# Kernel optimization log

Hardware: AMD Instinct MI355X
Metric: run time of the kernel (lower is better)

The kernel has to match this reference:

```python
import jax, jax.numpy as jnp
import numpy as np

B, T = 4, 2048
N_EMBD = 1024
TIME_EMBD = 128
N_HEAD = 16
C_IN = N_EMBD + TIME_EMBD  # 1152


def setup_inputs() -> dict:
    key = jax.random.key(0)
    ks = jax.random.split(key, 7)
    s_in = 1.0 / np.sqrt(C_IN)
    s_e = 1.0 / np.sqrt(N_EMBD)
    return {
        "x": jax.random.normal(ks[0], (B, T, C_IN), jnp.float32),
        "ln_w": jnp.ones((C_IN,), jnp.float32),
        "ln_b": jnp.zeros((C_IN,), jnp.float32),
        "W_attn": jax.random.normal(ks[1], (C_IN, 3 * N_EMBD), jnp.float32) * s_in,
        "b_attn": jax.random.normal(ks[2], (3 * N_EMBD,), jnp.float32) * 0.01,
        "W_proj": jax.random.normal(ks[3], (N_EMBD, N_EMBD), jnp.float32) * s_e,
        "b_proj": jax.random.normal(ks[4], (N_EMBD,), jnp.float32) * 0.01,
    }


def _layernorm(x, w, b, eps=1e-5):
    mu = jnp.mean(x, axis=-1, keepdims=True)
    var = jnp.var(x, axis=-1, keepdims=True)
    return (x - mu) * jax.lax.rsqrt(var + eps) * w + b


def reference(x, ln_w, ln_b, W_attn, b_attn, W_proj, b_proj):
    h = _layernorm(x, ln_w, ln_b)                      # [B,T,C_IN]
    qkv = h @ W_attn + b_attn                          # [B,T,3*N_EMBD]
    q, k, v = jnp.split(qkv, 3, axis=-1)
    hd = N_EMBD // N_HEAD
    q = q.reshape(B, T, N_HEAD, hd).transpose(0, 2, 1, 3)  # [B,H,T,hd]
    k = k.reshape(B, T, N_HEAD, hd).transpose(0, 2, 1, 3)
    v = v.reshape(B, T, N_HEAD, hd).transpose(0, 2, 1, 3)
    att = jnp.einsum("bhqd,bhkd->bhqk", q, k) * (1.0 / np.sqrt(hd))
    mask = jnp.tril(jnp.ones((T, T), bool))
    att = jnp.where(mask, att, -jnp.inf)
    att = jax.nn.softmax(att, axis=-1)                 # dropout p=0 -> identity
    y = jnp.einsum("bhqk,bhkd->bhqd", att, v)          # [B,H,T,hd]
    y = y.transpose(0, 2, 1, 3).reshape(B, T, N_EMBD)
    return y @ W_proj + b_proj
```

## Files before the change

kernel.cpp:

```cpp
#include <hip/hip_runtime.h>
#include <hip/hip_bf16.h>

#define BB 4
#define TT 2048
#define C_IN 1152
#define NE 1024
#define NH 16
#define HD 64
#define MM (BB*TT)
#define N_QKV (3*NE)

typedef __attribute__((ext_vector_type(8))) short s16x8;
typedef __attribute__((ext_vector_type(4))) float f32x4;

static __device__ __forceinline__ unsigned short f2bf(float x) {
    unsigned int u = __float_as_uint(x);
    unsigned int r = (u + 0x7fffu + ((u >> 16) & 1u)) >> 16;
    return (unsigned short)r;
}

static __device__ __forceinline__ void async16(const void* g, void* l) {
    __builtin_amdgcn_global_load_lds((const __attribute__((address_space(1))) void*)g,
                                     (__attribute__((address_space(3))) void*)l, 16, 0, 0);
}

__global__ __launch_bounds__(256) void ln_kernel(const float* __restrict__ x,
                                                 const float* __restrict__ w,
                                                 const float* __restrict__ b,
                                                 unsigned short* __restrict__ h) {
    const int row = blockIdx.x;
    const float* xr = x + (size_t)row * C_IN;
    float s = 0.f, sq = 0.f;
    for (int i = threadIdx.x; i < C_IN; i += 256) {
        float v = xr[i];
        s += v; sq += v * v;
    }
    for (int off = 1; off < 64; off <<= 1) {
        s  += __shfl_xor(s, off, 64);
        sq += __shfl_xor(sq, off, 64);
    }
    __shared__ float red[2][4];
    const int wid = threadIdx.x >> 6, lane = threadIdx.x & 63;
    if (lane == 0) { red[0][wid] = s; red[1][wid] = sq; }
    __syncthreads();
    s  = red[0][0] + red[0][1] + red[0][2] + red[0][3];
    sq = red[1][0] + red[1][1] + red[1][2] + red[1][3];
    const float mu  = s * (1.f / C_IN);
    const float var = sq * (1.f / C_IN) - mu * mu;
    const float rs  = rsqrtf(var + 1e-5f);
    unsigned short* hr = h + (size_t)row * C_IN;
    for (int i = threadIdx.x; i < C_IN; i += 256) {
        float v = (xr[i] - mu) * rs * w[i] + b[i];
        hr[i] = f2bf(v);
    }
}

__global__ __launch_bounds__(256) void transpose_cast(const float* __restrict__ in,
                                                      unsigned short* __restrict__ out,
                                                      int K, int N) {
    __shared__ float tile[32][33];
    const int n0 = blockIdx.x * 32, k0 = blockIdx.y * 32;
    const int tx = threadIdx.x & 31, ty = threadIdx.x >> 5;
    for (int i = ty; i < 32; i += 8)
        tile[i][tx] = in[(size_t)(k0 + i) * N + n0 + tx];
    __syncthreads();
    for (int i = ty; i < 32; i += 8)
        out[(size_t)(n0 + i) * K + k0 + tx] = f2bf(tile[tx][i]);
}

#define ATT_SC 0.18033688011112042f

#define EP_STRIDE 136
template <int MODE>
__global__ __launch_bounds__(256) void gemm_bt(const unsigned short* __restrict__ A,
                                               const unsigned short* __restrict__ Bt,
                                               const float* __restrict__ bias,
                                               void* __restrict__ outp,
                                               unsigned short* __restrict__ kb,
                                               unsigned short* __restrict__ vt,
                                               int M, int N, int K) {
    __shared__ unsigned short smem[16384];
    unsigned short* As = smem;
    unsigned short* Bs = smem + 8192;
    const int tid = threadIdx.x;
    const int wid = tid >> 6, lane = tid & 63;
    const int wm = wid >> 1, wn = wid & 1;
    const int quad = lane >> 4, l16 = lane & 15;
    const int m0 = blockIdx.y * 128, n0 = blockIdx.x * 128;

    const int srow = wid * 32 + (lane >> 2);
    const int scol = (lane & 3) * 8;
    const unsigned short* gA = A  + (size_t)(m0 + srow) * K + scol;
    const unsigned short* gB = Bt + (size_t)(n0 + srow) * K + scol;
    const int lofs = (wid * 32) * 32;

    f32x4 acc[4][4] = {};

    async16(gA,          &As[lofs]);
    async16(gA + 16 * K, &As[lofs + 16 * 32]);
    async16(gB,          &Bs[lofs]);
    async16(gB + 16 * K, &Bs[lofs + 16 * 32]);

    const int nk = K >> 5;
    for (int kt = 0; kt < nk; kt++) {
        __syncthreads();
        const int cur = kt & 1;
        if (kt + 1 < nk) {
            const int kk = (kt + 1) << 5;
            const int nxt = (cur ^ 1) * 4096;
            async16(gA + kk,          &As[nxt + lofs]);
            async16(gA + kk + 16 * K, &As[nxt + lofs + 16 * 32]);
            async16(gB + kk,          &Bs[nxt + lofs]);
            async16(gB + kk + 16 * K, &Bs[nxt + lofs + 16 * 32]);
        }
        const int cb = cur * 4096;
        s16x8 af[4], bfb[4];
        for (int mi = 0; mi < 4; mi++)
            af[mi] = *(const s16x8*)&As[cb + (wm * 64 + mi * 16 + l16) * 32 + quad * 8];
        for (int ni = 0; ni < 4; ni++)
            bfb[ni] = *(const s16x8*)&Bs[cb + (wn * 64 + ni * 16 + l16) * 32 + quad * 8];
        for (int mi = 0; mi < 4; mi++)
            for (int ni = 0; ni < 4; ni++)
                acc[mi][ni] = __builtin_amdgcn_mfma_f32_16x16x32_bf16(af[mi], bfb[ni], acc[mi][ni], 0, 0, 0);
    }

    const int which0 = n0 >> 10;
    const float sc = (MODE == 0 && which0 == 0) ? ATT_SC : 1.0f;
    for (int ni = 0; ni < 4; ni++) {
        const float bv = bias[n0 + wn * 64 + ni * 16 + l16];
        for (int mi = 0; mi < 4; mi++)
            for (int r = 0; r < 4; r++)
                acc[mi][ni][r] = (acc[mi][ni][r] + bv) * sc;
    }

    if (MODE == 1) {
        for (int mi = 0; mi < 4; mi++) {
            const int mbase = m0 + wm * 64 + mi * 16 + quad * 4;
            for (int ni = 0; ni < 4; ni++) {
                const int n_g = n0 + wn * 64 + ni * 16 + l16;
                for (int r = 0; r < 4; r++)
                    ((float*)outp)[(size_t)(mbase + r) * N + n_g] = acc[mi][ni][r];
            }
        }
        return;
    }

    const int which = n0 >> 10;
    const int bb = m0 >> 11;
    const int mloc = m0 & 2047;
    unsigned short* T = smem;

    if (which < 2) {
        unsigned short* qk = (which == 0) ? (unsigned short*)outp : kb;
        for (int pass = 0; pass < 2; pass++) {
            __syncthreads();
            if (wm == pass) {
                for (int mi = 0; mi < 4; mi++)
                    for (int ni = 0; ni < 4; ni++) {
                        const int nl = wn * 64 + ni * 16 + l16;
                        for (int r = 0; r < 4; r++)
                            T[(mi * 16 + quad * 4 + r) * EP_STRIDE + nl] = f2bf(acc[mi][ni][r]);
                    }
            }
            __syncthreads();
            const int ml = tid >> 2, c = tid & 3;
            const int t  = mloc + pass * 64 + ml;
            const int nl0 = c * 32;
            const int hh = ((n0 & 1023) >> 6) + (nl0 >> 6);
            const int d0 = nl0 & 63;
            unsigned short* dst = qk + ((size_t)(bb * 16 + hh) * TT + t) * HD + d0;
            const unsigned short* src = &T[ml * EP_STRIDE + nl0];
            for (int u = 0; u < 4; u++)
                *(s16x8*)(dst + u * 8) = *(const s16x8*)(src + u * 8);
        }
    } else {
        for (int pass = 0; pass < 2; pass++) {
            __syncthreads();
            if (wn == pass) {
                for (int mi = 0; mi < 4; mi++)
                    for (int ni = 0; ni < 4; ni++) {
                        const int nlh = ni * 16 + l16;
                        const int mlb = wm * 64 + mi * 16 + quad * 4;
                        for (int r = 0; r < 4; r += 2) {
                            const unsigned int pk = (unsigned int)f2bf(acc[mi][ni][r]) |
                                                    ((unsigned int)f2bf(acc[mi][ni][r + 1]) << 16);
                            *(unsigned int*)&T[nlh * EP_STRIDE + mlb + r] = pk;
                        }
                    }
            }
            __syncthreads();
            const int nlh = tid >> 2, c = tid & 3;
            const int hh = (n0 - 2048 + pass * 64) >> 6;
            unsigned short* dst = vt + ((size_t)(bb * 16 + hh) * HD + nlh) * TT + mloc + c * 32;
            const unsigned short* src = &T[nlh * EP_STRIDE + c * 32];
            for (int u = 0; u < 4; u++)
                *(s16x8*)(dst + u * 8) = *(const s16x8*)(src + u * 8);
        }
    }
}

#define PST 72

__global__ __launch_bounds__(256) void attn_kernel(const unsigned short* __restrict__ qb,
                                                   const unsigned short* __restrict__ kb,
                                                   const unsigned short* __restrict__ vt,
                                                   unsigned short* __restrict__ yb) {
    __shared__ unsigned short Ks[2][64 * 64];
    __shared__ unsigned short Vs[2][64 * 64];
    __shared__ unsigned short Ps[4][2 * 16 * PST];
    const int tid = threadIdx.x, wid = tid >> 6, lane = tid & 63;
    const int quad = lane >> 4, l16 = lane & 15;
    const int bh = blockIdx.x & 63;
    const int qblk = 15 - (blockIdx.x >> 6);

    const unsigned short* qh = qb + (size_t)bh * TT * HD;
    const unsigned short* kh = kb + (size_t)bh * TT * HD;
    const unsigned short* vh = vt + (size_t)bh * HD * TT;
    unsigned short* ps = Ps[wid];

    const int q0w = qblk * 128 + wid * 32;
    s16x8 aq[2][2];
    #pragma unroll
    for (int mf = 0; mf < 2; mf++) {
        aq[mf][0] = *(const s16x8*)&qh[(size_t)(q0w + mf * 16 + l16) * HD + quad * 8];
        aq[mf][1] = *(const s16x8*)&qh[(size_t)(q0w + mf * 16 + l16) * HD + 32 + quad * 8];
    }
    s16x8 onesf;
    #pragma unroll
    for (int i = 0; i < 8; i++) onesf[i] = (short)0x3F80;

    f32x4 yacc[2][4] = {};
    f32x4 lacc[2] = {};
    const int ntiles = 2 * qblk + 2;

    const int rl = lane >> 3;
    const int cc = (lane & 7) ^ (rl & 7);
    const unsigned short* kp0 = kh + (size_t)(wid * 16 + rl) * HD + cc * 8;
    const unsigned short* kp1 = kh + (size_t)(wid * 16 + 8 + rl) * HD + cc * 8;
    const unsigned short* vp0 = vh + (size_t)(wid * 16 + rl) * TT + cc * 8;
    const unsigned short* vp1 = vh + (size_t)(wid * 16 + 8 + rl) * TT + cc * 8;
    const int ldsK0 = wid * 16 * 64, ldsK1 = (wid * 16 + 8) * 64;

    async16(kp0, &Ks[0][ldsK0]);  async16(kp1, &Ks[0][ldsK1]);
    async16(vp0, &Vs[0][ldsK0]);  async16(vp1, &Vs[0][ldsK1]);
    kp0 += 64 * HD; kp1 += 64 * HD; vp0 += 64; vp1 += 64;

    const int p0s = quad ^ (l16 & 7);
    const int p1s = (4 + quad) ^ (l16 & 7);

#define ATT_STEP(CUR, TT_)                                                              \
    {                                                                                   \
        __syncthreads();                                                                \
        if ((TT_) + 1 < ntiles) {                                                       \
            async16(kp0, &Ks[(CUR) ^ 1][ldsK0]);  async16(kp1, &Ks[(CUR) ^ 1][ldsK1]);  \
            async16(vp0, &Vs[(CUR) ^ 1][ldsK0]);  async16(vp1, &Vs[(CUR) ^ 1][ldsK1]);  \
            kp0 += 64 * HD; kp1 += 64 * HD; vp0 += 64; vp1 += 64;                       \
        }                                                                               \
        const int tk0 = (TT_) * 64;                                                     \
        if (tk0 <= q0w + 31) {                                                          \
            const unsigned short* Kc = Ks[CUR];                                         \
            const unsigned short* Vc = Vs[CUR];                                         \
            s16x8 kf[4][2], vf[4][2];                                                   \
            _Pragma("unroll")                                                           \
            for (int nj = 0; nj < 4; nj++) {                                            \
                kf[nj][0] = *(const s16x8*)&Kc[(nj * 16 + l16) * 64 + p0s * 8];         \
                kf[nj][1] = *(const s16x8*)&Kc[(nj * 16 + l16) * 64 + p1s * 8];         \
            }                                                                           \
            _Pragma("unroll")                                                           \
            for (int ni = 0; ni < 4; ni++) {                                            \
                vf[ni][0] = *(const s16x8*)&Vc[(ni * 16 + l16) * 64 + p0s * 8];         \
                vf[ni][1] = *(const s16x8*)&Vc[(ni * 16 + l16) * 64 + p1s * 8];         \
            }                                                                           \
            _Pragma("unroll")                                                           \
            for (int mf = 0; mf < 2; mf++) {                                            \
                const int f0 = q0w + mf * 16;                                           \
                if (tk0 > f0 + 15) continue;                                            \
                unsigned short* pm = ps + mf * (16 * PST);                              \
                const int qg = f0 + l16;                                                \
                f32x4 st[4];                                                            \
                _Pragma("unroll")                                                       \
                for (int nj = 0; nj < 4; nj++) {                                        \
                    f32x4 z = {};                                                       \
                    z = __builtin_amdgcn_mfma_f32_16x16x32_bf16(kf[nj][0], aq[mf][0], z, 0, 0, 0); \
                    z = __builtin_amdgcn_mfma_f32_16x16x32_bf16(kf[nj][1], aq[mf][1], z, 0, 0, 0); \
                    st[nj] = z;                                                         \
                }                                                                       \
                const bool diag = (tk0 + 64 > f0);                                      \
                _Pragma("unroll")                                                       \
                for (int nj = 0; nj < 4; nj++) {                                        \
                    const int keyb = tk0 + nj * 16 + quad * 4;                          \
                    float pv[4];                                                        \
                    _Pragma("unroll")                                                   \
                    for (int r = 0; r < 4; r++) {                                       \
                        float p = exp2f(st[nj][r]);                                     \
                        if (diag && (keyb + r > qg)) p = 0.f;                           \
                        pv[r] = p;                                                      \
                    }                                                                   \
                    const unsigned int pk0 = __builtin_amdgcn_perm(                     \
                        __float_as_uint(pv[1]), __float_as_uint(pv[0]), 0x07060302u);   \
                    const unsigned int pk1 = __builtin_amdgcn_perm(                     \
                        __float_as_uint(pv[3]), __float_as_uint(pv[2]), 0x07060302u);   \
                    *(uint2*)&pm[l16 * PST + nj * 16 + quad * 4] = make_uint2(pk0, pk1);\
                }                                                                       \
                __asm volatile("s_waitcnt lgkmcnt(0)" ::: "memory");                    \
                const s16x8 ap0 = *(const s16x8*)&pm[l16 * PST + quad * 8];             \
                const s16x8 ap1 = *(const s16x8*)&pm[l16 * PST + 32 + quad * 8];        \
                lacc[mf] = __builtin_amdgcn_mfma_f32_16x16x32_bf16(ap0, onesf, lacc[mf], 0, 0, 0); \
                lacc[mf] = __builtin_amdgcn_mfma_f32_16x16x32_bf16(ap1, onesf, lacc[mf], 0, 0, 0); \
                _Pragma("unroll")                                                       \
                for (int ni = 0; ni < 4; ni++) {                                        \
                    yacc[mf][ni] = __builtin_amdgcn_mfma_f32_16x16x32_bf16(ap0, vf[ni][0], yacc[mf][ni], 0, 0, 0); \
                    yacc[mf][ni] = __builtin_amdgcn_mfma_f32_16x16x32_bf16(ap1, vf[ni][1], yacc[mf][ni], 0, 0, 0); \
                }                                                                       \
            }                                                                           \
        }                                                                               \
    }

    for (int t = 0; t < ntiles; t += 2) {
        ATT_STEP(0, t);
        ATT_STEP(1, t + 1);
    }
#undef ATT_STEP

    const int bbi = bh >> 4, hh = bh & 15;
    #pragma unroll
    for (int mf = 0; mf < 2; mf++) {
        float linv[4];
        #pragma unroll
        for (int r = 0; r < 4; r++)
            linv[r] = 1.0f / lacc[mf][r];
        #pragma unroll
        for (int ni = 0; ni < 4; ni++)
            #pragma unroll
            for (int r = 0; r < 4; r++) {
                const int trow = q0w + mf * 16 + quad * 4 + r;
                yb[((size_t)bbi * TT + trow) * NE + hh * HD + ni * 16 + l16] =
                    f2bf(yacc[mf][ni][r] * linv[r]);
            }
    }
}

extern "C" void kernel_launch(void* const* d_in, const int* in_sizes, int n_in,
                              void* d_out, int out_size, void* d_ws, size_t ws_size,
                              hipStream_t stream) {
    const float* x      = (const float*)d_in[0];
    const float* ln_w   = (const float*)d_in[1];
    const float* ln_b   = (const float*)d_in[2];
    const float* W_attn = (const float*)d_in[3];
    const float* b_attn = (const float*)d_in[4];
    const float* W_proj = (const float*)d_in[5];
    const float* b_proj = (const float*)d_in[6];
    float* out = (float*)d_out;

    char* ws = (char*)d_ws;
    unsigned short* h    = (unsigned short*)ws;  ws += (size_t)MM * C_IN * 2;
    unsigned short* Wat  = (unsigned short*)ws;  ws += (size_t)N_QKV * C_IN * 2;
    unsigned short* Wpt  = (unsigned short*)ws;  ws += (size_t)NE * NE * 2;
    unsigned short* qbuf = (unsigned short*)ws;  ws += (size_t)MM * NE * 2;
    unsigned short* kbuf = (unsigned short*)ws;  ws += (size_t)MM * NE * 2;
    unsigned short* vtbf = (unsigned short*)ws;  ws += (size_t)MM * NE * 2;
    unsigned short* ybuf = (unsigned short*)ws;  ws += (size_t)MM * NE * 2;

    ln_kernel<<<MM, 256, 0, stream>>>(x, ln_w, ln_b, h);
    transpose_cast<<<dim3(N_QKV / 32, C_IN / 32), 256, 0, stream>>>(W_attn, Wat, C_IN, N_QKV);
    transpose_cast<<<dim3(NE / 32, NE / 32), 256, 0, stream>>>(W_proj, Wpt, NE, NE);
    gemm_bt<0><<<dim3(N_QKV / 128, MM / 128), 256, 0, stream>>>(h, Wat, b_attn, qbuf, kbuf, vtbf,
                                                                MM, N_QKV, C_IN);
    attn_kernel<<<64 * 16, 256, 0, stream>>>(qbuf, kbuf, vtbf, ybuf);
    gemm_bt<1><<<dim3(NE / 128, MM / 128), 256, 0, stream>>>(ybuf, Wpt, b_proj, out, nullptr, nullptr,
                                                             MM, NE, NE);
}
```

Before: 314.5 us.

## Replace GEMM with 256x256-tile, 512-thread kernel using a four-stage LDS ring

Both GEMMs move from a 128x128 tile with 256 threads and double buffering to a 256x256 tile with 8 waves. A four-slot LDS ring is filled two k-steps ahead, with explicit vmcnt waits and raw barriers in place of __syncthreads. LDS is laid out in MFMA fragment order so each lane reads contiguous 16-byte fragments, and the MFMA bursts are wrapped in s_setprio. The bias add and scaling move into the epilogue stores, which are widened to 256 columns. Each block now needs 128 KB of LDS, and the grids shrink to 384 and 128 blocks, which may leave CUs idle, especially in the output projection.

```diff
diff --git a/kernel.cpp b/kernel.cpp
--- a/kernel.cpp
+++ b/kernel.cpp
@@ -70,76 +70,96 @@
 
 #define ATT_SC 0.18033688011112042f
 
-#define EP_STRIDE 136
+#define EPAD 264
+
 template <int MODE>
-__global__ __launch_bounds__(256) void gemm_bt(const unsigned short* __restrict__ A,
-                                               const unsigned short* __restrict__ Bt,
-                                               const float* __restrict__ bias,
-                                               void* __restrict__ outp,
-                                               unsigned short* __restrict__ kb,
-                                               unsigned short* __restrict__ vt,
-                                               int M, int N, int K) {
-    __shared__ unsigned short smem[16384];
-    unsigned short* As = smem;
-    unsigned short* Bs = smem + 8192;
+__global__ __launch_bounds__(512, 2) void gemm_fm(const unsigned short* __restrict__ A,
+                                                  const unsigned short* __restrict__ Bt,
+                                                  const float* __restrict__ bias,
+                                                  void* __restrict__ outp,
+                                                  unsigned short* __restrict__ kb,
+                                                  unsigned short* __restrict__ vt,
+                                                  int M, int N, int K) {
+    __shared__ unsigned short sm[65536];
+    unsigned short* sA = sm;
+    unsigned short* sB = sm + 32768;
     const int tid = threadIdx.x;
-    const int wid = tid >> 6, lane = tid & 63;
-    const int wm = wid >> 1, wn = wid & 1;
+    const int lane = tid & 63, wid = tid >> 6;
+    const int wm = wid >> 2, wn = wid & 3;
     const int quad = lane >> 4, l16 = lane & 15;
-    const int m0 = blockIdx.y * 128, n0 = blockIdx.x * 128;
-
-    const int srow = wid * 32 + (lane >> 2);
-    const int scol = (lane & 3) * 8;
-    const unsigned short* gA = A  + (size_t)(m0 + srow) * K + scol;
-    const unsigned short* gB = Bt + (size_t)(n0 + srow) * K + scol;
-    const int lofs = (wid * 32) * 32;
-
-    f32x4 acc[4][4] = {};
-
-    async16(gA,          &As[lofs]);
-    async16(gA + 16 * K, &As[lofs + 16 * 32]);
-    async16(gB,          &Bs[lofs]);
-    async16(gB + 16 * K, &Bs[lofs + 16 * 32]);
-
+    const int m0 = blockIdx.y * 256, n0 = blockIdx.x * 256;
+
+    const unsigned short* gA0 = A  + (size_t)(m0 + wid * 16 + l16) * K + quad * 8;
+    const unsigned short* gB0 = Bt + (size_t)(n0 + wid * 16 + l16) * K + quad * 8;
+    const size_t j1 = (size_t)128 * K;
+    const int stA0 = wid * 512, stA1 = (8 + wid) * 512;
+
+    f32x4 acc[8][4] = {};
     const int nk = K >> 5;
-    for (int kt = 0; kt < nk; kt++) {
-        __syncthreads();
-        const int cur = kt & 1;
-        if (kt + 1 < nk) {
-            const int kk = (kt + 1) << 5;
-            const int nxt = (cur ^ 1) * 4096;
-            async16(gA + kk,          &As[nxt + lofs]);
-            async16(gA + kk + 16 * K, &As[nxt + lofs + 16 * 32]);
-            async16(gB + kk,          &Bs[nxt + lofs]);
-            async16(gB + kk + 16 * K, &Bs[nxt + lofs + 16 * 32]);
-        }
-        const int cb = cur * 4096;
-        s16x8 af[4], bfb[4];
+
+    async16(gA0,           &sA[stA0]);          async16(gA0 + j1,      &sA[stA1]);
+    async16(gB0,           &sB[stA0]);          async16(gB0 + j1,      &sB[stA1]);
+    async16(gA0 + 32,      &sA[8192 + stA0]);   async16(gA0 + j1 + 32, &sA[8192 + stA1]);
+    async16(gB0 + 32,      &sB[8192 + stA0]);   async16(gB0 + j1 + 32, &sB[8192 + stA1]);
+
+    for (int kt = 0; kt < nk; ++kt) {
+        const int cb = (kt & 3) * 8192;
+        if (kt + 1 < nk) { asm volatile("s_waitcnt vmcnt(4)" ::: "memory"); }
+        else             { asm volatile("s_waitcnt vmcnt(0)" ::: "memory"); }
+        __builtin_amdgcn_s_barrier();
+
+        const int pre = kt + 2;
+        const bool do_pre = (pre < nk);
+        const int pb = (pre & 3) * 8192;
+        const unsigned short* pA = gA0 + pre * 32;
+        const unsigned short* pB = gB0 + pre * 32;
+
+        s16x8 af[4], bf[4];
+        #pragma unroll
+        for (int i = 0; i < 4; i++)
+            af[i] = *(const s16x8*)&sA[cb + (wm * 8 + i) * 512 + lane * 8];
+        #pragma unroll
+        for (int i = 0; i < 4; i++)
+            bf[i] = *(const s16x8*)&sB[cb + (wn * 4 + i) * 512 + lane * 8];
+        if (do_pre) { async16(pA, &sA[pb + stA0]); async16(pA + j1, &sA[pb + stA1]); }
+        __builtin_amdgcn_s_setprio(1);
+        #pragma unroll
         for (int mi = 0; mi < 4; mi++)
-            af[mi] = *(const s16x8*)&As[cb + (wm * 64 + mi * 16 + l16) * 32 + quad * 8];
-        for (int ni = 0; ni < 4; ni++)
-            bfb[ni] = *(const s16x8*)&Bs[cb + (wn * 64 + ni * 16 + l16) * 32 + quad * 8];
+            #pragma unroll
+            for (int ni = 0; ni < 4; ni++)
+                acc[mi][ni] = __builtin_amdgcn_mfma_f32_16x16x32_bf16(af[mi], bf[ni], acc[mi][ni], 0, 0, 0);
+        __builtin_amdgcn_s_setprio(0);
+        __builtin_amdgcn_s_barrier();
+
+        #pragma unroll
+        for (int i = 0; i < 4; i++)
+            af[i] = *(const s16x8*)&sA[cb + (wm * 8 + 4 + i) * 512 + lane * 8];
+        if (do_pre) { async16(pB, &sB[pb + stA0]); async16(pB + j1, &sB[pb + stA1]); }
+        __builtin_amdgcn_s_setprio(1);
+        #pragma unroll
         for (int mi = 0; mi < 4; mi++)
+            #pragma unroll
             for (int ni = 0; ni < 4; ni++)
-                acc[mi][ni] = __builtin_amdgcn_mfma_f32_16x16x32_bf16(af[mi], bfb[ni], acc[mi][ni], 0, 0, 0);
-    }
-
-    const int which0 = n0 >> 10;
-    const float sc = (MODE == 0 && which0 == 0) ? ATT_SC : 1.0f;
-    for (int ni = 0; ni < 4; ni++) {
-        const float bv = bias[n0 + wn * 64 + ni * 16 + l16];
-        for (int mi = 0; mi < 4; mi++)
-            for (int r = 0; r < 4; r++)
-                acc[mi][ni][r] = (acc[mi][ni][r] + bv) * sc;
-    }
+                acc[4 + mi][ni] = __builtin_amdgcn_mfma_f32_16x16x32_bf16(af[mi], bf[ni], acc[4 + mi][ni], 0, 0, 0);
+        __builtin_amdgcn_s_setprio(0);
+    }
+
+    float bv[4];
+    #pragma unroll
+    for (int ni = 0; ni < 4; ni++)
+        bv[ni] = bias[n0 + wn * 64 + ni * 16 + l16];
 
     if (MODE == 1) {
-        for (int mi = 0; mi < 4; mi++) {
-            const int mbase = m0 + wm * 64 + mi * 16 + quad * 4;
+        float* out = (float*)outp;
+        #pragma unroll
+        for (int mf = 0; mf < 8; mf++) {
+            const int mg = m0 + wm * 128 + mf * 16 + quad * 4;
+            #pragma unroll
             for (int ni = 0; ni < 4; ni++) {
-                const int n_g = n0 + wn * 64 + ni * 16 + l16;
+                const int ng = n0 + wn * 64 + ni * 16 + l16;
+                #pragma unroll
                 for (int r = 0; r < 4; r++)
-                    ((float*)outp)[(size_t)(mbase + r) * N + n_g] = acc[mi][ni][r];
+                    out[(size_t)(mg + r) * N + ng] = acc[mf][ni][r] + bv[ni];
             }
         }
         return;
@@ -148,53 +168,65 @@
     const int which = n0 >> 10;
     const int bb = m0 >> 11;
     const int mloc = m0 & 2047;
-    unsigned short* T = smem;
+    const float sc = (which == 0) ? ATT_SC : 1.0f;
+    unsigned short* T = sm;
 
     if (which < 2) {
         unsigned short* qk = (which == 0) ? (unsigned short*)outp : kb;
-        for (int pass = 0; pass < 2; pass++) {
+        const int hb = (n0 & 1023) >> 6;
+        for (int p = 0; p < 4; p++) {
             __syncthreads();
-            if (wm == pass) {
-                for (int mi = 0; mi < 4; mi++)
+            if (wm == (p >> 1)) {
+                #pragma unroll
+                for (int i = 0; i < 4; i++) {
+                    const int mf = (p & 1) * 4 + i;
+                    #pragma unroll
                     for (int ni = 0; ni < 4; ni++) {
-                        const int nl = wn * 64 + ni * 16 + l16;
+                        const int col = wn * 64 + ni * 16 + l16;
+                        #pragma unroll
                         for (int r = 0; r < 4; r++)
-                            T[(mi * 16 + quad * 4 + r) * EP_STRIDE + nl] = f2bf(acc[mi][ni][r]);
+                            T[(i * 16 + quad * 4 + r) * EPAD + col] =
+                                f2bf((acc[mf][ni][r] + bv[ni]) * sc);
                     }
+                }
             }
             __syncthreads();
-            const int ml = tid >> 2, c = tid & 3;
-            const int t  = mloc + pass * 64 + ml;
-            const int nl0 = c * 32;
-            const int hh = ((n0 & 1023) >> 6) + (nl0 >> 6);
-            const int d0 = nl0 & 63;
-            unsigned short* dst = qk + ((size_t)(bb * 16 + hh) * TT + t) * HD + d0;
-            const unsigned short* src = &T[ml * EP_STRIDE + nl0];
-            for (int u = 0; u < 4; u++)
-                *(s16x8*)(dst + u * 8) = *(const s16x8*)(src + u * 8);
+            const int c0 = (tid & 31) * 8;
+            const int hh = hb + (c0 >> 6), d0 = c0 & 63;
+            for (int rr = tid >> 5; rr < 64; rr += 16) {
+                const int t = mloc + p * 64 + rr;
+                *(s16x8*)(qk + ((size_t)(bb * 16 + hh) * TT + t) * HD + d0) =
+                    *(const s16x8*)&T[rr * EPAD + c0];
+            }
         }
     } else {
-        for (int pass = 0; pass < 2; pass++) {
+        const int hb = (n0 - 2048) >> 6;
+        for (int p = 0; p < 4; p++) {
             __syncthreads();
-            if (wn == pass) {
-                for (int mi = 0; mi < 4; mi++)
+            if (wn == p) {
+                #pragma unroll
+                for (int mf = 0; mf < 8; mf++) {
+                    const int colb = wm * 128 + mf * 16 + quad * 4;
+                    #pragma unroll
                     for (int ni = 0; ni < 4; ni++) {
-                        const int nlh = ni * 16 + l16;
-                        const int mlb = wm * 64 + mi * 16 + quad * 4;
-                        for (int r = 0; r < 4; r += 2) {
-                            const unsigned int pk = (unsigned int)f2bf(acc[mi][ni][r]) |
-                                                    ((unsigned int)f2bf(acc[mi][ni][r + 1]) << 16);
-                            *(unsigned int*)&T[nlh * EP_STRIDE + mlb + r] = pk;
-                        }
+                        const int rowt = ni * 16 + l16;
+                        const unsigned int pk0 =
+                            (unsigned int)f2bf(acc[mf][ni][0] + bv[ni]) |
+                            ((unsigned int)f2bf(acc[mf][ni][1] + bv[ni]) << 16);
+                        const unsigned int pk1 =
+                            (unsigned int)f2bf(acc[mf][ni][2] + bv[ni]) |
+                            ((unsigned int)f2bf(acc[mf][ni][3] + bv[ni]) << 16);
+                        *(unsigned int*)&T[rowt * EPAD + colb]     = pk0;
+                        *(unsigned int*)&T[rowt * EPAD + colb + 2] = pk1;
                     }
+                }
             }
             __syncthreads();
-            const int nlh = tid >> 2, c = tid & 3;
-            const int hh = (n0 - 2048 + pass * 64) >> 6;
-            unsigned short* dst = vt + ((size_t)(bb * 16 + hh) * HD + nlh) * TT + mloc + c * 32;
-            const unsigned short* src = &T[nlh * EP_STRIDE + c * 32];
-            for (int u = 0; u < 4; u++)
-                *(s16x8*)(dst + u * 8) = *(const s16x8*)(src + u * 8);
+            const int c0 = (tid & 31) * 8;
+            for (int dr = tid >> 5; dr < 64; dr += 16) {
+                *(s16x8*)(vt + ((size_t)(bb * 16 + hb + p) * HD + dr) * TT + mloc + c0) =
+                    *(const s16x8*)&T[dr * EPAD + c0];
+            }
         }
     }
 }
@@ -364,9 +396,9 @@
     ln_kernel<<<MM, 256, 0, stream>>>(x, ln_w, ln_b, h);
     transpose_cast<<<dim3(N_QKV / 32, C_IN / 32), 256, 0, stream>>>(W_attn, Wat, C_IN, N_QKV);
     transpose_cast<<<dim3(NE / 32, NE / 32), 256, 0, stream>>>(W_proj, Wpt, NE, NE);
-    gemm_bt<0><<<dim3(N_QKV / 128, MM / 128), 256, 0, stream>>>(h, Wat, b_attn, qbuf, kbuf, vtbf,
+    gemm_fm<0><<<dim3(N_QKV / 256, MM / 256), 512, 0, stream>>>(h, Wat, b_attn, qbuf, kbuf, vtbf,
                                                                 MM, N_QKV, C_IN);
     attn_kernel<<<64 * 16, 256, 0, stream>>>(qbuf, kbuf, vtbf, ybuf);
-    gemm_bt<1><<<dim3(NE / 128, MM / 128), 256, 0, stream>>>(ybuf, Wpt, b_proj, out, nullptr, nullptr,
+    gemm_fm<1><<<dim3(NE / 256, MM / 256), 512, 0, stream>>>(ybuf, Wpt, b_proj, out, nullptr, nullptr,
                                                              MM, NE, NE);
 }
```

Measured after the change: 375.6 us. 1.19x slower.

## Triple-buffer attention K/V loads, remap GEMM block order, raise MFMA priority

Applied to the files above, without the earlier changes.

Attention now keeps three K/V LDS buffers with two tiles prefetched ahead. Each step waits with an explicit vmcnt plus a raw s_barrier instead of __syncthreads, so global-load latency is better hidden behind compute. The P-matrix writes for both query fragments happen before the PV MFMAs, which run at raised wave priority. Separately, the GEMM remaps block IDs in an XCD-interleaved order to improve L2 locality across chiplets; the cost is more LDS per attention block, which may lower occupancy.

```diff
diff --git a/kernel.cpp b/kernel.cpp
--- a/kernel.cpp
+++ b/kernel.cpp
@@ -86,7 +86,12 @@
     const int wid = tid >> 6, lane = tid & 63;
     const int wm = wid >> 1, wn = wid & 1;
     const int quad = lane >> 4, l16 = lane & 15;
-    const int m0 = blockIdx.y * 128, n0 = blockIdx.x * 128;
+
+    const int gx  = gridDim.x;
+    const int nwg = gx * gridDim.y;
+    const int bid = blockIdx.y * gx + blockIdx.x;
+    const int wg  = (bid & 7) * (nwg >> 3) + (bid >> 3);
+    const int m0 = (wg / gx) * 128, n0 = (wg % gx) * 128;
 
     const int srow = wid * 32 + (lane >> 2);
     const int scol = (lane & 3) * 8;
@@ -205,8 +210,8 @@
                                                    const unsigned short* __restrict__ kb,
                                                    const unsigned short* __restrict__ vt,
                                                    unsigned short* __restrict__ yb) {
-    __shared__ unsigned short Ks[2][64 * 64];
-    __shared__ unsigned short Vs[2][64 * 64];
+    __shared__ unsigned short Ks[3][64 * 64];
+    __shared__ unsigned short Vs[3][64 * 64];
     __shared__ unsigned short Ps[4][2 * 16 * PST];
     const int tid = threadIdx.x, wid = tid >> 6, lane = tid & 63;
     const int quad = lane >> 4, l16 = lane & 15;
@@ -244,83 +249,89 @@
     async16(kp0, &Ks[0][ldsK0]);  async16(kp1, &Ks[0][ldsK1]);
     async16(vp0, &Vs[0][ldsK0]);  async16(vp1, &Vs[0][ldsK1]);
     kp0 += 64 * HD; kp1 += 64 * HD; vp0 += 64; vp1 += 64;
+    async16(kp0, &Ks[1][ldsK0]);  async16(kp1, &Ks[1][ldsK1]);
+    async16(vp0, &Vs[1][ldsK0]);  async16(vp1, &Vs[1][ldsK1]);
+    kp0 += 64 * HD; kp1 += 64 * HD; vp0 += 64; vp1 += 64;
 
     const int p0s = quad ^ (l16 & 7);
     const int p1s = (4 + quad) ^ (l16 & 7);
 
-#define ATT_STEP(CUR, TT_)                                                              \
-    {                                                                                   \
-        __syncthreads();                                                                \
-        if ((TT_) + 1 < ntiles) {                                                       \
-            async16(kp0, &Ks[(CUR) ^ 1][ldsK0]);  async16(kp1, &Ks[(CUR) ^ 1][ldsK1]);  \
-            async16(vp0, &Vs[(CUR) ^ 1][ldsK0]);  async16(vp1, &Vs[(CUR) ^ 1][ldsK1]);  \
-            kp0 += 64 * HD; kp1 += 64 * HD; vp0 += 64; vp1 += 64;                       \
-        }                                                                               \
-        const int tk0 = (TT_) * 64;                                                     \
-        if (tk0 <= q0w + 31) {                                                          \
-            const unsigned short* Kc = Ks[CUR];                                         \
-            const unsigned short* Vc = Vs[CUR];                                         \
-            s16x8 kf[4][2], vf[4][2];                                                   \
-            _Pragma("unroll")                                                           \
-            for (int nj = 0; nj < 4; nj++) {                                            \
-                kf[nj][0] = *(const s16x8*)&Kc[(nj * 16 + l16) * 64 + p0s * 8];         \
-                kf[nj][1] = *(const s16x8*)&Kc[(nj * 16 + l16) * 64 + p1s * 8];         \
-            }                                                                           \
-            _Pragma("unroll")                                                           \
-            for (int ni = 0; ni < 4; ni++) {                                            \
-                vf[ni][0] = *(const s16x8*)&Vc[(ni * 16 + l16) * 64 + p0s * 8];         \
-                vf[ni][1] = *(const s16x8*)&Vc[(ni * 16 + l16) * 64 + p1s * 8];         \
-            }                                                                           \
-            _Pragma("unroll")                                                           \
-            for (int mf = 0; mf < 2; mf++) {                                            \
-                const int f0 = q0w + mf * 16;                                           \
-                if (tk0 > f0 + 15) continue;                                            \
-                unsigned short* pm = ps + mf * (16 * PST);                              \
-                const int qg = f0 + l16;                                                \
-                f32x4 st[4];                                                            \
-                _Pragma("unroll")                                                       \
-                for (int nj = 0; nj < 4; nj++) {                                        \
-                    f32x4 z = {};                                                       \
-                    z = __builtin_amdgcn_mfma_f32_16x16x32_bf16(kf[nj][0], aq[mf][0], z, 0, 0, 0); \
-                    z = __builtin_amdgcn_mfma_f32_16x16x32_bf16(kf[nj][1], aq[mf][1], z, 0, 0, 0); \
-                    st[nj] = z;                                                         \
-                }                                                                       \
-                const bool diag = (tk0 + 64 > f0);                                      \
-                _Pragma("unroll")                                                       \
-                for (int nj = 0; nj < 4; nj++) {                                        \
-                    const int keyb = tk0 + nj * 16 + quad * 4;                          \
-                    float pv[4];                                                        \
-                    _Pragma("unroll")                                                   \
-                    for (int r = 0; r < 4; r++) {                                       \
-                        float p = exp2f(st[nj][r]);                                     \
-                        if (diag && (keyb + r > qg)) p = 0.f;                           \
-                        pv[r] = p;                                                      \
-                    }                                                                   \
-                    const unsigned int pk0 = __builtin_amdgcn_perm(                     \
-                        __float_as_uint(pv[1]), __float_as_uint(pv[0]), 0x07060302u);   \
-                    const unsigned int pk1 = __builtin_amdgcn_perm(                     \
-                        __float_as_uint(pv[3]), __float_as_uint(pv[2]), 0x07060302u);   \
-                    *(uint2*)&pm[l16 * PST + nj * 16 + quad * 4] = make_uint2(pk0, pk1);\
-                }                                                                       \
-                __asm volatile("s_waitcnt lgkmcnt(0)" ::: "memory");                    \
-                const s16x8 ap0 = *(const s16x8*)&pm[l16 * PST + quad * 8];             \
-                const s16x8 ap1 = *(const s16x8*)&pm[l16 * PST + 32 + quad * 8];        \
-                lacc[mf] = __builtin_amdgcn_mfma_f32_16x16x32_bf16(ap0, onesf, lacc[mf], 0, 0, 0); \
-                lacc[mf] = __builtin_amdgcn_mfma_f32_16x16x32_bf16(ap1, onesf, lacc[mf], 0, 0, 0); \
-                _Pragma("unroll")                                                       \
-                for (int ni = 0; ni < 4; ni++) {                                        \
-                    yacc[mf][ni] = __builtin_amdgcn_mfma_f32_16x16x32_bf16(ap0, vf[ni][0], yacc[mf][ni], 0, 0, 0); \
-                    yacc[mf][ni] = __builtin_amdgcn_mfma_f32_16x16x32_bf16(ap1, vf[ni][1], yacc[mf][ni], 0, 0, 0); \
-                }                                                                       \
-            }                                                                           \
-        }                                                                               \
-    }
-
-    for (int t = 0; t < ntiles; t += 2) {
-        ATT_STEP(0, t);
-        ATT_STEP(1, t + 1);
-    }
-#undef ATT_STEP
+    int bsel = 0;
+    for (int t = 0; t < ntiles; ++t) {
+        if (t + 1 < ntiles) { asm volatile("s_waitcnt vmcnt(4)" ::: "memory"); }
+        else                { asm volatile("s_waitcnt vmcnt(0)" ::: "memory"); }
+        __builtin_amdgcn_s_barrier();
+        if (t + 2 < ntiles) {
+            const int wsel = (bsel == 0) ? 2 : bsel - 1;
+            async16(kp0, &Ks[wsel][ldsK0]);  async16(kp1, &Ks[wsel][ldsK1]);
+            async16(vp0, &Vs[wsel][ldsK0]);  async16(vp1, &Vs[wsel][ldsK1]);
+            kp0 += 64 * HD; kp1 += 64 * HD; vp0 += 64; vp1 += 64;
+        }
+        const int tk0 = t * 64;
+        if (tk0 <= q0w + 31) {
+            const unsigned short* Kc = Ks[bsel];
+            const unsigned short* Vc = Vs[bsel];
+            s16x8 kf[4][2], vf[4][2];
+            #pragma unroll
+            for (int nj = 0; nj < 4; nj++) {
+                kf[nj][0] = *(const s16x8*)&Kc[(nj * 16 + l16) * 64 + p0s * 8];
+                kf[nj][1] = *(const s16x8*)&Kc[(nj * 16 + l16) * 64 + p1s * 8];
+            }
+            #pragma unroll
+            for (int ni = 0; ni < 4; ni++) {
+                vf[ni][0] = *(const s16x8*)&Vc[(ni * 16 + l16) * 64 + p0s * 8];
+                vf[ni][1] = *(const s16x8*)&Vc[(ni * 16 + l16) * 64 + p1s * 8];
+            }
+            #pragma unroll
+            for (int mf = 0; mf < 2; mf++) {
+                const int f0 = q0w + mf * 16;
+                unsigned short* pm = ps + mf * (16 * PST);
+                const int qg = f0 + l16;
+                f32x4 st[4];
+                #pragma unroll
+                for (int nj = 0; nj < 4; nj++) {
+                    f32x4 z = {};
+                    z = __builtin_amdgcn_mfma_f32_16x16x32_bf16(kf[nj][0], aq[mf][0], z, 0, 0, 0);
+                    z = __builtin_amdgcn_mfma_f32_16x16x32_bf16(kf[nj][1], aq[mf][1], z, 0, 0, 0);
+                    st[nj] = z;
+                }
+                const bool diag = (tk0 + 64 > f0);
+                #pragma unroll
+                for (int nj = 0; nj < 4; nj++) {
+                    const int keyb = tk0 + nj * 16 + quad * 4;
+                    float pv[4];
+                    #pragma unroll
+                    for (int r = 0; r < 4; r++) {
+                        float p = exp2f(st[nj][r]);
+                        if (diag && (keyb + r > qg)) p = 0.f;
+                        pv[r] = p;
+                    }
+                    const unsigned int pk0 = __builtin_amdgcn_perm(
+                        __float_as_uint(pv[1]), __float_as_uint(pv[0]), 0x07060302u);
+                    const unsigned int pk1 = __builtin_amdgcn_perm(
+                        __float_as_uint(pv[3]), __float_as_uint(pv[2]), 0x07060302u);
+                    *(uint2*)&pm[l16 * PST + nj * 16 + quad * 4] = make_uint2(pk0, pk1);
+                }
+            }
+            __asm volatile("s_waitcnt lgkmcnt(0)" ::: "memory");
+            __builtin_amdgcn_s_setprio(1);
+            #pragma unroll
+            for (int mf = 0; mf < 2; mf++) {
+                unsigned short* pm = ps + mf * (16 * PST);
+                const s16x8 ap0 = *(const s16x8*)&pm[l16 * PST + quad * 8];
+                const s16x8 ap1 = *(const s16x8*)&pm[l16 * PST + 32 + quad * 8];
+                lacc[mf] = __builtin_amdgcn_mfma_f32_16x16x32_bf16(ap0, onesf, lacc[mf], 0, 0, 0);
+                lacc[mf] = __builtin_amdgcn_mfma_f32_16x16x32_bf16(ap1, onesf, lacc[mf], 0, 0, 0);
+                #pragma unroll
+                for (int ni = 0; ni < 4; ni++) {
+                    yacc[mf][ni] = __builtin_amdgcn_mfma_f32_16x16x32_bf16(ap0, vf[ni][0], yacc[mf][ni], 0, 0, 0);
+                    yacc[mf][ni] = __builtin_amdgcn_mfma_f32_16x16x32_bf16(ap1, vf[ni][1], yacc[mf][ni], 0, 0, 0);
+                }
+            }
+            __builtin_amdgcn_s_setprio(0);
+        }
+        bsel = (bsel == 2) ? 0 : bsel + 1;
+    }
 
     const int bbi = bh >> 4, hh = bh & 15;
     #pragma unroll
```

Measured after the change: 310.6 us. About the same (-1.2%).
